# Kernel optimization log

Hardware: AMD Instinct MI355X
Metric: run time of the kernel (lower is better)

The kernel has to match this reference:

```python
import jax, jax.numpy as jnp
from jax import lax
import numpy as np

T, B, INPUT_SIZE, HIDDEN, LAYERS, OUT_DIM = 256, 1000, 300, 2, 2, 1


def setup_inputs() -> dict:
    key = jax.random.key(0)
    ks = jax.random.split(key, 12)
    H4 = 4 * HIDDEN
    s = 0.1
    return {
        "x": jax.random.normal(ks[0], (T, B, INPUT_SIZE), dtype=jnp.float32),
        "h0": jnp.zeros((LAYERS, B, HIDDEN), dtype=jnp.float32),
        "c0": jnp.zeros((LAYERS, B, HIDDEN), dtype=jnp.float32),
        "W_ih0": jax.random.normal(ks[1], (H4, INPUT_SIZE), dtype=jnp.float32) * s,
        "W_hh0": jax.random.normal(ks[2], (H4, HIDDEN), dtype=jnp.float32) * s,
        "b_ih0": jax.random.normal(ks[3], (H4,), dtype=jnp.float32) * s,
        "b_hh0": jax.random.normal(ks[4], (H4,), dtype=jnp.float32) * s,
        "W_ih1": jax.random.normal(ks[5], (H4, HIDDEN), dtype=jnp.float32) * s,
        "W_hh1": jax.random.normal(ks[6], (H4, HIDDEN), dtype=jnp.float32) * s,
        "b_ih1": jax.random.normal(ks[7], (H4,), dtype=jnp.float32) * s,
        "b_hh1": jax.random.normal(ks[8], (H4,), dtype=jnp.float32) * s,
        "W_lin": jax.random.normal(ks[9], (OUT_DIM, HIDDEN), dtype=jnp.float32) * s,
        "b_lin": jax.random.normal(ks[10], (OUT_DIM,), dtype=jnp.float32) * s,
    }


def _lstm_layer(x, h0, c0, W_ih, W_hh, b_ih, b_hh):
    # x: [T, B, D_in]; PyTorch gate order i, f, g, o.
    # Precompute input projections for all timesteps at once (one big GEMM).
    xg = jnp.einsum('tbd,gd->tbg', x, W_ih) + (b_ih + b_hh)  # [T, B, 4H]

    def step(carry, xt):
        h, c = carry
        gates = xt + h @ W_hh.T  # [B, 4H]
        i, f, g, o = jnp.split(gates, 4, axis=-1)
        c = jax.nn.sigmoid(f) * c + jax.nn.sigmoid(i) * jnp.tanh(g)
        h = jax.nn.sigmoid(o) * jnp.tanh(c)
        return (h, c), h

    (_, _), ys = lax.scan(step, (h0, c0), xg)
    return ys  # [T, B, H]


def reference(x, h0, c0, W_ih0, W_hh0, b_ih0, b_hh0, W_ih1, W_hh1, b_ih1, b_hh1, W_lin, b_lin):
    y0 = _lstm_layer(x, h0[0], c0[0], W_ih0, W_hh0, b_ih0, b_hh0)   # [T, B, H]
    y1 = _lstm_layer(y0, h0[1], c0[1], W_ih1, W_hh1, b_ih1, b_hh1)  # [T, B, H]
    pred = y1[-1] @ W_lin.T + b_lin  # [B, 1]
    return pred.reshape(-1)          # [B]
```

## Files before the change

kernel.cpp:

```cpp
#include <hip/hip_runtime.h>

#define T_STEPS 256
#define BATCH   1000
#define D_IN    300
#define H4      8
#define NF4     75
#define RPB     128
#define NBLK    2000

#define L2E   1.4426950408889634f
#define L2E2  2.8853900817779268f

__device__ __forceinline__ float fexp2(float x) {
#if __has_builtin(__builtin_amdgcn_exp2f)
    return __builtin_amdgcn_exp2f(x);
#else
    return exp2f(x);
#endif
}
__device__ __forceinline__ float sig2(float x) {
    return __builtin_amdgcn_rcpf(1.0f + fexp2(-x));
}
__device__ __forceinline__ float tanh2(float x) {
    return fmaf(-2.0f, __builtin_amdgcn_rcpf(1.0f + fexp2(x)), 1.0f);
}

__device__ __forceinline__ float dot4acc(float4 a, float4 b, float acc) {
    return fmaf(a.x, b.x, fmaf(a.y, b.y, fmaf(a.z, b.z, fmaf(a.w, b.w, acc))));
}

__device__ __forceinline__ float swap1(float x) {
#if __has_builtin(__builtin_amdgcn_mov_dpp)
    return __int_as_float(
        __builtin_amdgcn_mov_dpp(__float_as_int(x), 0xB1, 0xF, 0xF, true));
#else
    return __shfl_xor(x, 1);
#endif
}

__global__ __launch_bounds__(256) void xproj_kernel(
    const float* __restrict__ x, const float* __restrict__ W,
    const float* __restrict__ b_ih, const float* __restrict__ b_hh,
    float* __restrict__ xg)
{
    __shared__ __align__(16) float4 ws4[H4 * NF4];

    const int tid = threadIdx.x;
    const float4* __restrict__ w4 = (const float4*)W;
    for (int k = tid; k < H4 * NF4; k += 256)
        ws4[k] = w4[k];
    __syncthreads();

    const int  lane = tid & 3;
    const int  quad = tid >> 2;
    const long row0 = (long)blockIdx.x * RPB + (long)quad * 2;

    const float4* __restrict__ x0 = (const float4*)x + row0 * NF4;
    const float4* __restrict__ x1 = x0 + NF4;

    float acc0[H4], acc1[H4];
#pragma unroll
    for (int g = 0; g < H4; ++g) { acc0[g] = 0.f; acc1[g] = 0.f; }

#pragma unroll 3
    for (int i = 0; i < 18; ++i) {
        const int k = 4 * i + lane;
        float4 xa = x0[k];
        float4 xb = x1[k];
#pragma unroll
        for (int g = 0; g < H4; ++g) {
            float4 wv = ws4[g * NF4 + k];
            acc0[g] = dot4acc(xa, wv, acc0[g]);
            acc1[g] = dot4acc(xb, wv, acc1[g]);
        }
    }
    {
        const int k = 72 + lane;
        if (k < NF4) {
            float4 xa = x0[k];
            float4 xb = x1[k];
#pragma unroll
            for (int g = 0; g < H4; ++g) {
                float4 wv = ws4[g * NF4 + k];
                acc0[g] = dot4acc(xa, wv, acc0[g]);
                acc1[g] = dot4acc(xb, wv, acc1[g]);
            }
        }
    }

#pragma unroll
    for (int g = 0; g < H4; ++g) {
        acc0[g] += __shfl_xor(acc0[g], 1);
        acc0[g] += __shfl_xor(acc0[g], 2);
        acc1[g] += __shfl_xor(acc1[g], 1);
        acc1[g] += __shfl_xor(acc1[g], 2);
    }

    const float b0 = b_ih[2 * lane]     + b_hh[2 * lane];
    const float b1 = b_ih[2 * lane + 1] + b_hh[2 * lane + 1];
    const float sc = (lane == 2) ? L2E2 : L2E;

    xg[row0 * 8 + lane]           = (acc0[2 * lane]     + b0) * sc;
    xg[row0 * 8 + 4 + lane]       = (acc0[2 * lane + 1] + b1) * sc;
    xg[(row0 + 1) * 8 + lane]     = (acc1[2 * lane]     + b0) * sc;
    xg[(row0 + 1) * 8 + 4 + lane] = (acc1[2 * lane + 1] + b1) * sc;
}

__global__ __launch_bounds__(64) void lstm_seq_kernel(
    const float* __restrict__ xg,
    const float* __restrict__ h0in, const float* __restrict__ c0in,
    const float* __restrict__ Whh0, const float* __restrict__ Wih1,
    const float* __restrict__ Whh1, const float* __restrict__ bih1,
    const float* __restrict__ bhh1, const float* __restrict__ Wlin,
    const float* __restrict__ blin, float* __restrict__ out)
{
    const int gid   = blockIdx.x * 64 + threadIdx.x;
    const int e_raw = gid >> 1;
    const int u     = gid & 1;
    const bool wr   = (e_raw < BATCH) && (u == 0);
    const int  e    = (e_raw < BATCH) ? e_raw : (BATCH - 1);

    float wa0[4], wb0[4], wa1i[4], wb1i[4], wa1h[4], wb1h[4], bs1[4];
#pragma unroll
    for (int s = 0; s < 4; ++s) {
        const int   row = 2 * s + u;
        const float f   = (s == 2) ? L2E2 : L2E;
        wa0[s]  = Whh0[row * 2 + u]       * f;
        wb0[s]  = Whh0[row * 2 + (1 - u)] * f;
        wa1i[s] = Wih1[row * 2 + u]       * f;
        wb1i[s] = Wih1[row * 2 + (1 - u)] * f;
        wa1h[s] = Whh1[row * 2 + u]       * f;
        wb1h[s] = Whh1[row * 2 + (1 - u)] * f;
        bs1[s]  = (bih1[row] + bhh1[row]) * f;
    }

    float h0 = h0in[2 * e + u];
    float c0 = c0in[2 * e + u];
    float h1 = h0in[2 * BATCH + 2 * e + u];
    float c1 = c0in[2 * BATCH + 2 * e + u];

    const float4* __restrict__ xq = (const float4*)xg;
    float4 pre[4];
#pragma unroll
    for (int t = 0; t < 4; ++t)
        pre[t] = xq[((long)t * BATCH + e) * 2 + u];

    float h1o = swap1(h1);
    float p[4];
#pragma unroll
    for (int s = 0; s < 4; ++s)
        p[s] = bs1[s] + h1 * wa1h[s] + h1o * wb1h[s];

#pragma unroll 4
    for (int t = 0; t < T_STEPS; ++t) {
        const int sl = t & 3;
        const float4 xv = pre[sl];
        if (t + 4 < T_STEPS)
            pre[sl] = xq[((long)(t + 4) * BATCH + e) * 2 + u];

        const float h0o = swap1(h0);
        const float gi = xv.x + h0 * wa0[0] + h0o * wb0[0];
        const float gf = xv.y + h0 * wa0[1] + h0o * wb0[1];
        const float gg = xv.z + h0 * wa0[2] + h0o * wb0[2];
        const float go = xv.w + h0 * wa0[3] + h0o * wb0[3];
        c0 = sig2(gf) * c0 + sig2(gi) * tanh2(gg);
        h0 = sig2(go) * tanh2(c0 * L2E2);

        const float h0n = swap1(h0);
        const float qi = p[0] + h0 * wa1i[0] + h0n * wb1i[0];
        const float qf = p[1] + h0 * wa1i[1] + h0n * wb1i[1];
        const float qg = p[2] + h0 * wa1i[2] + h0n * wb1i[2];
        const float qo = p[3] + h0 * wa1i[3] + h0n * wb1i[3];
        c1 = sig2(qf) * c1 + sig2(qi) * tanh2(qg);
        h1 = sig2(qo) * tanh2(c1 * L2E2);

        const float h1n = swap1(h1);
#pragma unroll
        for (int s = 0; s < 4; ++s)
            p[s] = bs1[s] + h1 * wa1h[s] + h1n * wb1h[s];
    }

    const float h1b = swap1(h1);
    if (wr)
        out[e] = h1 * Wlin[0] + h1b * Wlin[1] + blin[0];
}

extern "C" void kernel_launch(void* const* d_in, const int* in_sizes, int n_in,
                              void* d_out, int out_size, void* d_ws, size_t ws_size,
                              hipStream_t stream) {
    const float* x      = (const float*)d_in[0];
    const float* h0     = (const float*)d_in[1];
    const float* c0     = (const float*)d_in[2];
    const float* W_ih0  = (const float*)d_in[3];
    const float* W_hh0  = (const float*)d_in[4];
    const float* b_ih0  = (const float*)d_in[5];
    const float* b_hh0  = (const float*)d_in[6];
    const float* W_ih1  = (const float*)d_in[7];
    const float* W_hh1  = (const float*)d_in[8];
    const float* b_ih1  = (const float*)d_in[9];
    const float* b_hh1  = (const float*)d_in[10];
    const float* W_lin  = (const float*)d_in[11];
    const float* b_lin  = (const float*)d_in[12];
    float* out = (float*)d_out;
    float* xg  = (float*)d_ws;

    xproj_kernel<<<NBLK, 256, 0, stream>>>(x, W_ih0, b_ih0, b_hh0, xg);
    lstm_seq_kernel<<<(2 * BATCH + 63) / 64, 64, 0, stream>>>(
        xg, h0, c0, W_hh0, W_ih1, W_hh1, b_ih1, b_hh1, W_lin, b_lin, out);
}
```

Baseline: 498.5 us.

## Fuse input projection and recurrence into one producer-consumer persistent kernel

Merges the input-projection GEMM and the sequential LSTM recurrence into a single launch. 512 producer blocks compute projection tiles and publish per-tile flags with release stores. 8 consumer blocks poll those flags with a wavefront ballot before loading each group of four timesteps. The aim is to overlap the bandwidth-bound projection with the latency-bound recurrence and to drop one kernel launch. In exchange it adds a memset and flag-polling overhead, and consumers can only make progress if producer and consumer blocks are resident at the same time.

Result: slower. 582.8 us (+16.9%).

```diff
diff --git a/kernel.cpp b/kernel.cpp
--- a/kernel.cpp
+++ b/kernel.cpp
@@ -6,7 +6,10 @@
 #define H4      8
 #define NF4     75
 #define RPB     128
-#define NBLK    2000
+#define NTILE   2000
+#define NPROD   512
+#define NCONS   8
+#define GOLDEN  0x3A701B4D
 
 #define L2E   1.4426950408889634f
 #define L2E2  2.8853900817779268f
@@ -24,11 +27,9 @@
 __device__ __forceinline__ float tanh2(float x) {
     return fmaf(-2.0f, __builtin_amdgcn_rcpf(1.0f + fexp2(x)), 1.0f);
 }
-
 __device__ __forceinline__ float dot4acc(float4 a, float4 b, float acc) {
     return fmaf(a.x, b.x, fmaf(a.y, b.y, fmaf(a.z, b.z, fmaf(a.w, b.w, acc))));
 }
-
 __device__ __forceinline__ float swap1(float x) {
 #if __has_builtin(__builtin_amdgcn_mov_dpp)
     return __int_as_float(
@@ -37,152 +38,197 @@
     return __shfl_xor(x, 1);
 #endif
 }
-
-__global__ __launch_bounds__(256) void xproj_kernel(
+__device__ __forceinline__ void acq_fence() {
+#if __has_builtin(__builtin_amdgcn_fence)
+    __builtin_amdgcn_fence(__ATOMIC_ACQUIRE, "agent");
+#else
+    __threadfence();
+#endif
+}
+
+__device__ __forceinline__ void ensure(int need, int& F, int& granted,
+                                       const int* flags, int lane) {
+    if (granted >= need) return;
+    while (granted < need) {
+        int idx = F + lane;
+        if (idx >= NTILE) idx = NTILE - 1;
+        int v = __hip_atomic_load(&flags[idx], __ATOMIC_RELAXED,
+                                  __HIP_MEMORY_SCOPE_AGENT);
+        unsigned long long nm = ~__ballot(v == GOLDEN);
+        int adv = nm ? (int)__builtin_ctzll(nm) : 64;
+        if (adv == 0) __builtin_amdgcn_s_sleep(8);
+        F += adv;
+        if (F > NTILE) F = NTILE;
+        granted = (F * RPB) / BATCH;
+    }
+    acq_fence();
+}
+
+__global__ __launch_bounds__(256) void fused_kernel(
     const float* __restrict__ x, const float* __restrict__ W,
     const float* __restrict__ b_ih, const float* __restrict__ b_hh,
-    float* __restrict__ xg)
-{
-    __shared__ __align__(16) float4 ws4[H4 * NF4];
-
-    const int tid = threadIdx.x;
-    const float4* __restrict__ w4 = (const float4*)W;
-    for (int k = tid; k < H4 * NF4; k += 256)
-        ws4[k] = w4[k];
-    __syncthreads();
-
-    const int  lane = tid & 3;
-    const int  quad = tid >> 2;
-    const long row0 = (long)blockIdx.x * RPB + (long)quad * 2;
-
-    const float4* __restrict__ x0 = (const float4*)x + row0 * NF4;
-    const float4* __restrict__ x1 = x0 + NF4;
-
-    float acc0[H4], acc1[H4];
-#pragma unroll
-    for (int g = 0; g < H4; ++g) { acc0[g] = 0.f; acc1[g] = 0.f; }
-
-#pragma unroll 3
-    for (int i = 0; i < 18; ++i) {
-        const int k = 4 * i + lane;
-        float4 xa = x0[k];
-        float4 xb = x1[k];
-#pragma unroll
-        for (int g = 0; g < H4; ++g) {
-            float4 wv = ws4[g * NF4 + k];
-            acc0[g] = dot4acc(xa, wv, acc0[g]);
-            acc1[g] = dot4acc(xb, wv, acc1[g]);
-        }
-    }
-    {
-        const int k = 72 + lane;
-        if (k < NF4) {
-            float4 xa = x0[k];
-            float4 xb = x1[k];
-#pragma unroll
-            for (int g = 0; g < H4; ++g) {
-                float4 wv = ws4[g * NF4 + k];
-                acc0[g] = dot4acc(xa, wv, acc0[g]);
-                acc1[g] = dot4acc(xb, wv, acc1[g]);
-            }
-        }
-    }
-
-#pragma unroll
-    for (int g = 0; g < H4; ++g) {
-        acc0[g] += __shfl_xor(acc0[g], 1);
-        acc0[g] += __shfl_xor(acc0[g], 2);
-        acc1[g] += __shfl_xor(acc1[g], 1);
-        acc1[g] += __shfl_xor(acc1[g], 2);
-    }
-
-    const float b0 = b_ih[2 * lane]     + b_hh[2 * lane];
-    const float b1 = b_ih[2 * lane + 1] + b_hh[2 * lane + 1];
-    const float sc = (lane == 2) ? L2E2 : L2E;
-
-    xg[row0 * 8 + lane]           = (acc0[2 * lane]     + b0) * sc;
-    xg[row0 * 8 + 4 + lane]       = (acc0[2 * lane + 1] + b1) * sc;
-    xg[(row0 + 1) * 8 + lane]     = (acc1[2 * lane]     + b0) * sc;
-    xg[(row0 + 1) * 8 + 4 + lane] = (acc1[2 * lane + 1] + b1) * sc;
-}
-
-__global__ __launch_bounds__(64) void lstm_seq_kernel(
-    const float* __restrict__ xg,
     const float* __restrict__ h0in, const float* __restrict__ c0in,
     const float* __restrict__ Whh0, const float* __restrict__ Wih1,
     const float* __restrict__ Whh1, const float* __restrict__ bih1,
     const float* __restrict__ bhh1, const float* __restrict__ Wlin,
-    const float* __restrict__ blin, float* __restrict__ out)
+    const float* __restrict__ blin,
+    float* __restrict__ xg, int* flags,
+    float* __restrict__ out)
 {
-    const int gid   = blockIdx.x * 64 + threadIdx.x;
-    const int e_raw = gid >> 1;
-    const int u     = gid & 1;
-    const bool wr   = (e_raw < BATCH) && (u == 0);
-    const int  e    = (e_raw < BATCH) ? e_raw : (BATCH - 1);
-
-    float wa0[4], wb0[4], wa1i[4], wb1i[4], wa1h[4], wb1h[4], bs1[4];
-#pragma unroll
-    for (int s = 0; s < 4; ++s) {
-        const int   row = 2 * s + u;
-        const float f   = (s == 2) ? L2E2 : L2E;
-        wa0[s]  = Whh0[row * 2 + u]       * f;
-        wb0[s]  = Whh0[row * 2 + (1 - u)] * f;
-        wa1i[s] = Wih1[row * 2 + u]       * f;
-        wb1i[s] = Wih1[row * 2 + (1 - u)] * f;
-        wa1h[s] = Whh1[row * 2 + u]       * f;
-        wb1h[s] = Whh1[row * 2 + (1 - u)] * f;
-        bs1[s]  = (bih1[row] + bhh1[row]) * f;
+    __shared__ __align__(16) float4 ws4[H4 * NF4];
+
+    if (blockIdx.x < NPROD) {
+        const int tid = threadIdx.x;
+        const float4* __restrict__ w4 = (const float4*)W;
+        for (int k = tid; k < H4 * NF4; k += 256)
+            ws4[k] = w4[k];
+        __syncthreads();
+
+        const int  lane = tid & 3;
+        const int  quad = tid >> 2;
+        const float b0 = b_ih[2 * lane]     + b_hh[2 * lane];
+        const float b1 = b_ih[2 * lane + 1] + b_hh[2 * lane + 1];
+        const float sc = (lane == 2) ? L2E2 : L2E;
+
+        for (int tile = blockIdx.x; tile < NTILE; tile += NPROD) {
+            const long row0 = (long)tile * RPB + (long)quad * 2;
+            const float4* __restrict__ x0 = (const float4*)x + row0 * NF4;
+            const float4* __restrict__ x1 = x0 + NF4;
+
+            float acc0[H4], acc1[H4];
+#pragma unroll
+            for (int g = 0; g < H4; ++g) { acc0[g] = 0.f; acc1[g] = 0.f; }
+
+#pragma unroll 3
+            for (int i = 0; i < 18; ++i) {
+                const int k = 4 * i + lane;
+                float4 xa = x0[k];
+                float4 xb = x1[k];
+#pragma unroll
+                for (int g = 0; g < H4; ++g) {
+                    float4 wv = ws4[g * NF4 + k];
+                    acc0[g] = dot4acc(xa, wv, acc0[g]);
+                    acc1[g] = dot4acc(xb, wv, acc1[g]);
+                }
+            }
+            {
+                const int k = 72 + lane;
+                if (k < NF4) {
+                    float4 xa = x0[k];
+                    float4 xb = x1[k];
+#pragma unroll
+                    for (int g = 0; g < H4; ++g) {
+                        float4 wv = ws4[g * NF4 + k];
+                        acc0[g] = dot4acc(xa, wv, acc0[g]);
+                        acc1[g] = dot4acc(xb, wv, acc1[g]);
+                    }
+                }
+            }
+
+#pragma unroll
+            for (int g = 0; g < H4; ++g) {
+                acc0[g] += __shfl_xor(acc0[g], 1);
+                acc0[g] += __shfl_xor(acc0[g], 2);
+                acc1[g] += __shfl_xor(acc1[g], 1);
+                acc1[g] += __shfl_xor(acc1[g], 2);
+            }
+
+            xg[row0 * 8 + lane]           = (acc0[2 * lane]     + b0) * sc;
+            xg[row0 * 8 + 4 + lane]       = (acc0[2 * lane + 1] + b1) * sc;
+            xg[(row0 + 1) * 8 + lane]     = (acc1[2 * lane]     + b0) * sc;
+            xg[(row0 + 1) * 8 + 4 + lane] = (acc1[2 * lane + 1] + b1) * sc;
+
+            __syncthreads();
+            if (tid == 0)
+                __hip_atomic_store(&flags[tile], GOLDEN,
+                                   __ATOMIC_RELEASE, __HIP_MEMORY_SCOPE_AGENT);
+        }
+    } else {
+        const int cg    = (blockIdx.x - NPROD) * 256 + threadIdx.x;
+        const int e_raw = cg >> 1;
+        const int u     = cg & 1;
+        const bool wr   = (e_raw < BATCH) && (u == 0);
+        const int  e    = (e_raw < BATCH) ? e_raw : (BATCH - 1);
+        const int  lane = threadIdx.x & 63;
+
+        float wa0[4], wb0[4], wa1i[4], wb1i[4], wa1h[4], wb1h[4], bs1[4];
+#pragma unroll
+        for (int s = 0; s < 4; ++s) {
+            const int   row = 2 * s + u;
+            const float f   = (s == 2) ? L2E2 : L2E;
+            wa0[s]  = Whh0[row * 2 + u]       * f;
+            wb0[s]  = Whh0[row * 2 + (1 - u)] * f;
+            wa1i[s] = Wih1[row * 2 + u]       * f;
+            wb1i[s] = Wih1[row * 2 + (1 - u)] * f;
+            wa1h[s] = Whh1[row * 2 + u]       * f;
+            wb1h[s] = Whh1[row * 2 + (1 - u)] * f;
+            bs1[s]  = (bih1[row] + bhh1[row]) * f;
+        }
+
+        float h0 = h0in[2 * e + u];
+        float c0 = c0in[2 * e + u];
+        float h1 = h0in[2 * BATCH + 2 * e + u];
+        float c1 = c0in[2 * BATCH + 2 * e + u];
+
+        const float4* __restrict__ xq = (const float4*)xg;
+        const long base = (long)e * 2 + u;
+
+        float h1o = swap1(h1);
+        float p[4];
+#pragma unroll
+        for (int s = 0; s < 4; ++s)
+            p[s] = bs1[s] + h1 * wa1h[s] + h1o * wb1h[s];
+
+#define LSTEP(xv)                                                        \
+        {                                                                \
+            const float h0o = swap1(h0);                                 \
+            const float gi = (xv).x + h0 * wa0[0] + h0o * wb0[0];        \
+            const float gf = (xv).y + h0 * wa0[1] + h0o * wb0[1];        \
+            const float gg = (xv).z + h0 * wa0[2] + h0o * wb0[2];        \
+            const float go = (xv).w + h0 * wa0[3] + h0o * wb0[3];        \
+            c0 = sig2(gf) * c0 + sig2(gi) * tanh2(gg);                   \
+            h0 = sig2(go) * tanh2(c0 * L2E2);                            \
+            const float h0n = swap1(h0);                                 \
+            const float qi = p[0] + h0 * wa1i[0] + h0n * wb1i[0];        \
+            const float qf = p[1] + h0 * wa1i[1] + h0n * wb1i[1];        \
+            const float qg = p[2] + h0 * wa1i[2] + h0n * wb1i[2];        \
+            const float qo = p[3] + h0 * wa1i[3] + h0n * wb1i[3];        \
+            c1 = sig2(qf) * c1 + sig2(qi) * tanh2(qg);                   \
+            h1 = sig2(qo) * tanh2(c1 * L2E2);                            \
+            const float h1n = swap1(h1);                                 \
+            p[0] = bs1[0] + h1 * wa1h[0] + h1n * wb1h[0];                \
+            p[1] = bs1[1] + h1 * wa1h[1] + h1n * wb1h[1];                \
+            p[2] = bs1[2] + h1 * wa1h[2] + h1n * wb1h[2];                \
+            p[3] = bs1[3] + h1 * wa1h[3] + h1n * wb1h[3];                \
+        }
+
+        int F = 0, granted = 0;
+        ensure(4, F, granted, flags, lane);
+        float4 q0 = xq[(long)0 * 2 * BATCH + base];
+        float4 q1 = xq[(long)1 * 2 * BATCH + base];
+        float4 q2 = xq[(long)2 * 2 * BATCH + base];
+        float4 q3 = xq[(long)3 * 2 * BATCH + base];
+
+        for (int tb = 0; tb < T_STEPS; tb += 4) {
+            const bool more = (tb + 4) < T_STEPS;
+            float4 n0, n1, n2, n3;
+            if (more) {
+                int need = tb + 8; if (need > T_STEPS) need = T_STEPS;
+                ensure(need, F, granted, flags, lane);
+                n0 = xq[(long)(tb + 4) * 2 * BATCH + base];
+                n1 = xq[(long)(tb + 5) * 2 * BATCH + base];
+                n2 = xq[(long)(tb + 6) * 2 * BATCH + base];
+                n3 = xq[(long)(tb + 7) * 2 * BATCH + base];
+            }
+            LSTEP(q0); LSTEP(q1); LSTEP(q2); LSTEP(q3);
+            if (more) { q0 = n0; q1 = n1; q2 = n2; q3 = n3; }
+        }
+#undef LSTEP
+
+        const float h1b = swap1(h1);
+        if (wr)
+            out[e] = h1 * Wlin[0] + h1b * Wlin[1] + blin[0];
     }
-
-    float h0 = h0in[2 * e + u];
-    float c0 = c0in[2 * e + u];
-    float h1 = h0in[2 * BATCH + 2 * e + u];
-    float c1 = c0in[2 * BATCH + 2 * e + u];
-
-    const float4* __restrict__ xq = (const float4*)xg;
-    float4 pre[4];
-#pragma unroll
-    for (int t = 0; t < 4; ++t)
-        pre[t] = xq[((long)t * BATCH + e) * 2 + u];
-
-    float h1o = swap1(h1);
-    float p[4];
-#pragma unroll
-    for (int s = 0; s < 4; ++s)
-        p[s] = bs1[s] + h1 * wa1h[s] + h1o * wb1h[s];
-
-#pragma unroll 4
-    for (int t = 0; t < T_STEPS; ++t) {
-        const int sl = t & 3;
-        const float4 xv = pre[sl];
-        if (t + 4 < T_STEPS)
-            pre[sl] = xq[((long)(t + 4) * BATCH + e) * 2 + u];
-
-        const float h0o = swap1(h0);
-        const float gi = xv.x + h0 * wa0[0] + h0o * wb0[0];
-        const float gf = xv.y + h0 * wa0[1] + h0o * wb0[1];
-        const float gg = xv.z + h0 * wa0[2] + h0o * wb0[2];
-        const float go = xv.w + h0 * wa0[3] + h0o * wb0[3];
-        c0 = sig2(gf) * c0 + sig2(gi) * tanh2(gg);
-        h0 = sig2(go) * tanh2(c0 * L2E2);
-
-        const float h0n = swap1(h0);
-        const float qi = p[0] + h0 * wa1i[0] + h0n * wb1i[0];
-        const float qf = p[1] + h0 * wa1i[1] + h0n * wb1i[1];
-        const float qg = p[2] + h0 * wa1i[2] + h0n * wb1i[2];
-        const float qo = p[3] + h0 * wa1i[3] + h0n * wb1i[3];
-        c1 = sig2(qf) * c1 + sig2(qi) * tanh2(qg);
-        h1 = sig2(qo) * tanh2(c1 * L2E2);
-
-        const float h1n = swap1(h1);
-#pragma unroll
-        for (int s = 0; s < 4; ++s)
-            p[s] = bs1[s] + h1 * wa1h[s] + h1n * wb1h[s];
-    }
-
-    const float h1b = swap1(h1);
-    if (wr)
-        out[e] = h1 * Wlin[0] + h1b * Wlin[1] + blin[0];
 }
 
 extern "C" void kernel_launch(void* const* d_in, const int* in_sizes, int n_in,
@@ -202,9 +248,14 @@
     const float* W_lin  = (const float*)d_in[11];
     const float* b_lin  = (const float*)d_in[12];
     float* out = (float*)d_out;
-    float* xg  = (float*)d_ws;
-
-    xproj_kernel<<<NBLK, 256, 0, stream>>>(x, W_ih0, b_ih0, b_hh0, xg);
-    lstm_seq_kernel<<<(2 * BATCH + 63) / 64, 64, 0, stream>>>(
-        xg, h0, c0, W_hh0, W_ih1, W_hh1, b_ih1, b_hh1, W_lin, b_lin, out);
-}
+
+    float* xg    = (float*)d_ws;
+    int*   flags = (int*)((char*)d_ws
+                          + (size_t)T_STEPS * BATCH * H4 * sizeof(float));
+
+    hipMemsetAsync(flags, 0, NTILE * sizeof(int), stream);
+
+    fused_kernel<<<NPROD + NCONS, 256, 0, stream>>>(
+        x, W_ih0, b_ih0, b_hh0, h0, c0, W_hh0, W_ih1, W_hh1,
+        b_ih1, b_hh1, W_lin, b_lin, xg, flags, out);
+}
```
